# Performance work log

Hardware: AMD Instinct MI355X
Metric: run time of the kernel (lower is better)

Reference implementation:

```python
import jax, jax.numpy as jnp
import numpy as np

N = 50000   # nodes
E = 300000  # edges
D = 256     # emb_dim
L = 5       # num_layers
BN_EPS = 1e-5


def setup_inputs() -> dict:
    key = jax.random.key(0)
    ks = jax.random.split(key, 6)
    scale = 0.05
    return {
        "x": jax.random.normal(ks[0], (N, D), jnp.float32),
        "src": jax.random.randint(ks[1], (E,), 0, N, dtype=jnp.int32),
        "dst": jax.random.randint(ks[2], (E,), 0, N, dtype=jnp.int32),
        "W1": jax.random.normal(ks[3], (L, D, D), jnp.float32) * scale,
        "b1": jnp.zeros((L, D), jnp.float32),
        "g1": jnp.ones((L, D), jnp.float32),
        "bt1": jnp.zeros((L, D), jnp.float32),
        "W2": jax.random.normal(ks[4], (L, D, D), jnp.float32) * scale,
        "b2": jnp.zeros((L, D), jnp.float32),
        "eps": jnp.zeros((L,), jnp.float32),
        "bn_g": jnp.ones((L, D), jnp.float32),
        "bn_b": jnp.zeros((L, D), jnp.float32),
    }


def _bn(h, gamma, beta):
    # torch BatchNorm1d training-mode forward: biased batch stats over nodes
    mean = jnp.mean(h, axis=0)
    var = jnp.var(h, axis=0)
    return (h - mean) * jax.lax.rsqrt(var + BN_EPS) * gamma + beta


def reference(x, src, dst, W1, b1, g1, bt1, W2, b2, eps, bn_g, bn_b):
    h = x
    for l in range(L):
        # GINConv: gather relu(x[src]) -> scatter-sum to dst
        msg = jax.nn.relu(h[src])                          # [E, D]
        agg = jax.ops.segment_sum(msg, dst, num_segments=N)  # [N, D]
        z = (1.0 + eps[l]) * h + agg
        # mlp: Linear -> BN -> ReLU -> Linear
        z = z @ W1[l] + b1[l]
        z = jax.nn.relu(_bn(z, g1[l], bt1[l]))
        z = z @ W2[l] + b2[l]
        # per-layer BatchNorm; dropout is identity (eval / drop_ratio=0)
        z = _bn(z, bn_g[l], bn_b[l])
        if l < L - 1:
            z = jax.nn.relu(z)
        h = z
    return h  # JK='last'
```

## Files before the change

kernel.cpp:

```cpp
#include <hip/hip_runtime.h>
#include <hip/hip_bf16.h>

#define N_NODES 50000
#define N_EDGES 300000
#define DIM 256
#define MPAD 50048

typedef __attribute__((ext_vector_type(8))) _Float16 half8;
typedef __attribute__((ext_vector_type(4))) _Float16 half4;
typedef __attribute__((ext_vector_type(4))) float f32x4;

__device__ __forceinline__ void async16(const void* g, void* l) {
    __builtin_amdgcn_global_load_lds(
        (const __attribute__((address_space(1))) unsigned int*)g,
        (__attribute__((address_space(3))) unsigned int*)l, 16, 0, 0);
}

__device__ __forceinline__ void bn_finalize_thread(const float* __restrict__ st,
                                                   const float* __restrict__ g,
                                                   const float* __restrict__ beta,
                                                   float* scshL, int d, int n) {
    float s = 0.0f, sq = 0.0f;
#pragma unroll
    for (int r = 0; r < 8; r++) {
        s += st[r * 512 + d];
        sq += st[r * 512 + 256 + d];
    }
    float invn = 1.0f / (float)n;
    float mean = s * invn;
    float var = sq * invn - mean * mean;
    float inv = rsqrtf(var + 1e-5f);
    float scale = g[d] * inv;
    scshL[d] = scale;
    scshL[256 + d] = beta[d] - mean * scale;
}

__global__ __launch_bounds__(256) void hist_dst(const int* __restrict__ dst,
                                                int* __restrict__ deg, int E) {
    int e = blockIdx.x * blockDim.x + threadIdx.x;
    if (e < E) atomicAdd(&deg[dst[e]], 1);
}

__global__ __launch_bounds__(1024) void scan_blk(const int* __restrict__ deg,
                                                 int* __restrict__ ptr,
                                                 int* __restrict__ bsum, int n) {
    __shared__ int wsum[16];
    __shared__ int wpre[16];
    int tid = threadIdx.x;
    int i = blockIdx.x * 1024 + tid;
    int v = (i < n) ? deg[i] : 0;
    int lane = tid & 63, w = tid >> 6;
    int s = v;
#pragma unroll
    for (int off = 1; off < 64; off <<= 1) {
        int t = __shfl_up(s, off, 64);
        if (lane >= off) s += t;
    }
    if (lane == 63) wsum[w] = s;
    __syncthreads();
    if (tid < 16) {
        int acc = 0;
        for (int j = 0; j < tid; j++) acc += wsum[j];
        wpre[tid] = acc;
    }
    __syncthreads();
    int incl = s + wpre[w];
    if (i < n) ptr[i] = incl - v;
    if (tid == 1023) bsum[blockIdx.x] = incl;
}

__global__ __launch_bounds__(1024) void scan_add(int* __restrict__ ptr,
                                                 const int* __restrict__ bsum,
                                                 int* __restrict__ cursor,
                                                 int n, int E) {
    __shared__ int soff;
    int tid = threadIdx.x;
    if (tid < 64) {
        int v = (tid < (int)blockIdx.x) ? bsum[tid] : 0;
#pragma unroll
        for (int off = 32; off > 0; off >>= 1) v += __shfl_down(v, off, 64);
        if (tid == 0) soff = v;
    }
    __syncthreads();
    int i = blockIdx.x * 1024 + tid;
    if (i < n) {
        int val = ptr[i] + soff;
        ptr[i] = val;
        cursor[i] = val;
    }
    if (i == n) ptr[n] = E;
}

__global__ __launch_bounds__(256) void scatter_src(const int* __restrict__ src,
                                                   const int* __restrict__ dst,
                                                   int* __restrict__ cursor,
                                                   int* __restrict__ srcbuf, int E) {
    int e = blockIdx.x * blockDim.x + threadIdx.x;
    if (e < E) {
        int pos = atomicAdd(&cursor[dst[e]], 1);
        srcbuf[pos] = src[e];
    }
}

__global__ __launch_bounds__(256) void prep(const float* __restrict__ W1,
                                            const float* __restrict__ W2,
                                            _Float16* __restrict__ Wt,
                                            const float* __restrict__ x,
                                            _Float16* __restrict__ hb) {
    __shared__ float tile[64][65];
    int tid = threadIdx.x;
    if (blockIdx.x < 160) {
        int mat = blockIdx.x >> 4;
        int t = blockIdx.x & 15;
        int tr = t >> 2, tc = t & 3;
        const float* W = (mat < 5) ? (W1 + (size_t)mat * 65536)
                                   : (W2 + (size_t)(mat - 5) * 65536);
        int c = tid & 63, r0 = tid >> 6;
#pragma unroll 4
        for (int i = 0; i < 16; i++) {
            int r = r0 + i * 4;
            tile[r][c] = W[(size_t)(tr * 64 + r) * 256 + tc * 64 + c];
        }
        __syncthreads();
        _Float16* o = Wt + (size_t)mat * 65536;
#pragma unroll 4
        for (int i = 0; i < 16; i++) {
            int r = r0 + i * 4;
            o[(size_t)(tc * 64 + r) * 256 + tr * 64 + c] = (_Float16)tile[c][r];
        }
    } else {
        size_t i = (size_t)(blockIdx.x - 160) * 256 + tid;
        float4 v = ((const float4*)x)[i];
        half4 o;
        o.x = (_Float16)v.x; o.y = (_Float16)v.y;
        o.z = (_Float16)v.z; o.w = (_Float16)v.w;
        ((half4*)hb)[i] = o;
    }
}

__global__ __launch_bounds__(256) void gather_h(const _Float16* __restrict__ h,
                                                const int* __restrict__ ptr,
                                                const int* __restrict__ srcbuf,
                                                _Float16* __restrict__ z,
                                                const float* __restrict__ eps) {
    int node = blockIdx.x * 4 + (threadIdx.x >> 6);
    if (node >= N_NODES) return;
    int lane = threadIdx.x & 63;
    int beg = ptr[node], end = ptr[node + 1];
    float s = 1.0f + eps[0];
    half4 hv = ((const half4*)(h + (size_t)node * DIM))[lane];
    float a0 = (float)hv.x * s, a1 = (float)hv.y * s;
    float a2 = (float)hv.z * s, a3 = (float)hv.w * s;
    int e = beg;
    for (; e + 4 <= end; e += 4) {
        int s0 = srcbuf[e], s1 = srcbuf[e + 1], s2 = srcbuf[e + 2], s3 = srcbuf[e + 3];
        half4 v0 = ((const half4*)(h + (size_t)s0 * DIM))[lane];
        half4 v1 = ((const half4*)(h + (size_t)s1 * DIM))[lane];
        half4 v2 = ((const half4*)(h + (size_t)s2 * DIM))[lane];
        half4 v3 = ((const half4*)(h + (size_t)s3 * DIM))[lane];
        a0 += fmaxf((float)v0.x, 0.f) + fmaxf((float)v1.x, 0.f)
            + fmaxf((float)v2.x, 0.f) + fmaxf((float)v3.x, 0.f);
        a1 += fmaxf((float)v0.y, 0.f) + fmaxf((float)v1.y, 0.f)
            + fmaxf((float)v2.y, 0.f) + fmaxf((float)v3.y, 0.f);
        a2 += fmaxf((float)v0.z, 0.f) + fmaxf((float)v1.z, 0.f)
            + fmaxf((float)v2.z, 0.f) + fmaxf((float)v3.z, 0.f);
        a3 += fmaxf((float)v0.w, 0.f) + fmaxf((float)v1.w, 0.f)
            + fmaxf((float)v2.w, 0.f) + fmaxf((float)v3.w, 0.f);
    }
    for (; e < end; e++) {
        half4 v = ((const half4*)(h + (size_t)srcbuf[e] * DIM))[lane];
        a0 += fmaxf((float)v.x, 0.f); a1 += fmaxf((float)v.y, 0.f);
        a2 += fmaxf((float)v.z, 0.f); a3 += fmaxf((float)v.w, 0.f);
    }
    half4 o;
    o.x = (_Float16)a0; o.y = (_Float16)a1;
    o.z = (_Float16)a2; o.w = (_Float16)a3;
    ((half4*)(z + (size_t)node * DIM))[lane] = o;
}

__global__ __launch_bounds__(256) void gather_bn(const _Float16* __restrict__ C,
                                                 const int* __restrict__ ptr,
                                                 const int* __restrict__ srcbuf,
                                                 _Float16* __restrict__ z,
                                                 const float* __restrict__ scsh,
                                                 const float* __restrict__ eps,
                                                 int l) {
    int node = blockIdx.x * 4 + (threadIdx.x >> 6);
    if (node >= N_NODES) return;
    int lane = threadIdx.x & 63;
    float4 sc = ((const float4*)scsh)[lane];
    float4 sh = ((const float4*)(scsh + DIM))[lane];
    int beg = ptr[node], end = ptr[node + 1];
    float s = 1.0f + eps[l];
    half4 hv = ((const half4*)(C + (size_t)node * DIM))[lane];
    float a0 = s * fmaxf((float)hv.x * sc.x + sh.x, 0.f);
    float a1 = s * fmaxf((float)hv.y * sc.y + sh.y, 0.f);
    float a2 = s * fmaxf((float)hv.z * sc.z + sh.z, 0.f);
    float a3 = s * fmaxf((float)hv.w * sc.w + sh.w, 0.f);
    int e = beg;
    for (; e + 4 <= end; e += 4) {
        int s0 = srcbuf[e], s1 = srcbuf[e + 1], s2 = srcbuf[e + 2], s3 = srcbuf[e + 3];
        half4 v0 = ((const half4*)(C + (size_t)s0 * DIM))[lane];
        half4 v1 = ((const half4*)(C + (size_t)s1 * DIM))[lane];
        half4 v2 = ((const half4*)(C + (size_t)s2 * DIM))[lane];
        half4 v3 = ((const half4*)(C + (size_t)s3 * DIM))[lane];
        a0 += fmaxf((float)v0.x * sc.x + sh.x, 0.f) + fmaxf((float)v1.x * sc.x + sh.x, 0.f)
            + fmaxf((float)v2.x * sc.x + sh.x, 0.f) + fmaxf((float)v3.x * sc.x + sh.x, 0.f);
        a1 += fmaxf((float)v0.y * sc.y + sh.y, 0.f) + fmaxf((float)v1.y * sc.y + sh.y, 0.f)
            + fmaxf((float)v2.y * sc.y + sh.y, 0.f) + fmaxf((float)v3.y * sc.y + sh.y, 0.f);
        a2 += fmaxf((float)v0.z * sc.z + sh.z, 0.f) + fmaxf((float)v1.z * sc.z + sh.z, 0.f)
            + fmaxf((float)v2.z * sc.z + sh.z, 0.f) + fmaxf((float)v3.z * sc.z + sh.z, 0.f);
        a3 += fmaxf((float)v0.w * sc.w + sh.w, 0.f) + fmaxf((float)v1.w * sc.w + sh.w, 0.f)
            + fmaxf((float)v2.w * sc.w + sh.w, 0.f) + fmaxf((float)v3.w * sc.w + sh.w, 0.f);
    }
    for (; e < end; e++) {
        half4 v = ((const half4*)(C + (size_t)srcbuf[e] * DIM))[lane];
        a0 += fmaxf((float)v.x * sc.x + sh.x, 0.f);
        a1 += fmaxf((float)v.y * sc.y + sh.y, 0.f);
        a2 += fmaxf((float)v.z * sc.z + sh.z, 0.f);
        a3 += fmaxf((float)v.w * sc.w + sh.w, 0.f);
    }
    half4 o;
    o.x = (_Float16)a0; o.y = (_Float16)a1;
    o.z = (_Float16)a2; o.w = (_Float16)a3;
    ((half4*)(z + (size_t)node * DIM))[lane] = o;
}

#define GEMM_EPILOGUE                                                        \
    __syncthreads();                                                         \
    float* colsum = (float*)((char*)smem + 34816);                           \
    float* colsq = colsum + 128;                                             \
    if (tid < 128) { colsum[tid] = 0.0f; colsq[tid] = 0.0f; }                \
    _Float16* Cs = (_Float16*)smem;                                          \
    float bcol[4];                                                           \
    _Pragma("unroll")                                                        \
    for (int j = 0; j < 4; j++) bcol[j] = bias[col0 + wn + j * 16 + lrow];   \
    float csum[4] = {0.f, 0.f, 0.f, 0.f};                                    \
    float csq[4] = {0.f, 0.f, 0.f, 0.f};                                     \
    _Pragma("unroll")                                                        \
    for (int i = 0; i < 4; i++) {                                            \
        int rl = wm + i * 16 + quad * 4;                                     \
        _Pragma("unroll")                                                    \
        for (int j = 0; j < 4; j++) {                                        \
            int cl = wn + j * 16 + lrow;                                     \
            _Pragma("unroll")                                                \
            for (int r = 0; r < 4; r++) {                                    \
                float v = acc[i][j][r] + bcol[j];                            \
                Cs[(rl + r) * 136 + cl] = (_Float16)v;                       \
                if (row0 + rl + r < M) { csum[j] += v; csq[j] += v * v; }    \
            }                                                                \
        }                                                                    \
    }                                                                        \
    __syncthreads();                                                         \
    {                                                                        \
        int rgrp = lane >> 4, ch = lane & 15;                                \
        _Pragma("unroll")                                                    \
        for (int it = 0; it < 8; it++) {                                     \
            int row = wid * 32 + it * 4 + rgrp;                              \
            uint4 vv = *(const uint4*)(Cs + row * 136 + ch * 8);             \
            *(uint4*)(C + (size_t)(row0 + row) * DIM + col0 + ch * 8) = vv;  \
        }                                                                    \
    }                                                                        \
    _Pragma("unroll")                                                        \
    for (int j = 0; j < 4; j++) {                                            \
        atomicAdd(&colsum[wn + j * 16 + lrow], csum[j]);                     \
        atomicAdd(&colsq[wn + j * 16 + lrow], csq[j]);                       \
    }                                                                        \
    __syncthreads();                                                         \
    if (tid < 128) {                                                         \
        float* st = stats + (blockIdx.y & 7) * 512;                          \
        atomicAdd(&st[col0 + tid], colsum[tid]);                             \
        atomicAdd(&st[DIM + col0 + tid], colsq[tid]);                        \
    }

__global__ __launch_bounds__(256) void gemm_f16(const _Float16* __restrict__ A,
                                                const _Float16* __restrict__ Wt,
                                                const float* __restrict__ bias,
                                                _Float16* __restrict__ C,
                                                float* __restrict__ stats,
                                                int M) {
    __shared__ uint4 smem[2240];

    int tid = threadIdx.x;
    int wid = tid >> 6, lane = tid & 63;
    int quad = lane >> 4, lrow = lane & 15;
    int row0 = blockIdx.y * 128, col0 = blockIdx.x * 128;
    int wm = (wid & 1) * 64, wn = (wid >> 1) * 64;

    f32x4 acc[4][4] = {};
    const char* Ab = (const char*)A;
    const char* Bb = (const char*)Wt;

#pragma unroll
    for (int ko = 0; ko < 4; ko++) {
        int kb0 = ko * 128;
#pragma unroll
        for (int j = 0; j < 4; j++) {
            int sbase = wid * 256 + j * 64;
            int s = sbase + lane;
            int m = s >> 3;
            int c = (s & 7) ^ (m & 7);
            size_t go = (size_t)(row0 + m) * 512 + kb0 + c * 16;
            async16(Ab + go, (char*)smem + sbase * 16);
            size_t gob = (size_t)(col0 + m) * 512 + kb0 + c * 16;
            async16(Bb + gob, (char*)smem + 16384 + sbase * 16);
        }
        __syncthreads();
#pragma unroll
        for (int kc = 0; kc < 2; kc++) {
            half8 af[4], bf[4];
#pragma unroll
            for (int t = 0; t < 4; t++) {
                int ma = wm + t * 16 + lrow;
                int ca = kc * 4 + quad;
                af[t] = *(const half8*)((const char*)smem +
                                        (ma * 8 + (ca ^ (ma & 7))) * 16);
                int mb = wn + t * 16 + lrow;
                bf[t] = *(const half8*)((const char*)smem + 16384 +
                                        (mb * 8 + (ca ^ (mb & 7))) * 16);
            }
#pragma unroll
            for (int i = 0; i < 4; i++)
#pragma unroll
                for (int j2 = 0; j2 < 4; j2++)
                    acc[i][j2] = __builtin_amdgcn_mfma_f32_16x16x32_f16(
                        af[i], bf[j2], acc[i][j2], 0, 0, 0);
        }
        if (ko < 3) __syncthreads();
    }

    GEMM_EPILOGUE
}

__global__ __launch_bounds__(256) void gemm_bn(const _Float16* __restrict__ A,
                                               const _Float16* __restrict__ Wt,
                                               const float* __restrict__ bias,
                                               _Float16* __restrict__ C,
                                               float* __restrict__ stats,
                                               const float* __restrict__ statsIn,
                                               const float* __restrict__ gamma1,
                                               const float* __restrict__ beta1,
                                               int M) {
    __shared__ uint4 smem[2368];

    int tid = threadIdx.x;
    int wid = tid >> 6, lane = tid & 63;
    int quad = lane >> 4, lrow = lane & 15;
    int row0 = blockIdx.y * 128, col0 = blockIdx.x * 128;
    int wm = (wid & 1) * 64, wn = (wid >> 1) * 64;

    float* scshL = (float*)((char*)smem + 35840);
    bn_finalize_thread(statsIn, gamma1, beta1, scshL, tid, M);
    __syncthreads();

    half8 scv[8], shv[8];
#pragma unroll
    for (int cc = 0; cc < 8; cc++) {
        int kk = cc * 32 + quad * 8;
        float4 s0 = *(const float4*)(scshL + kk);
        float4 s1 = *(const float4*)(scshL + kk + 4);
        float4 h0 = *(const float4*)(scshL + DIM + kk);
        float4 h1 = *(const float4*)(scshL + DIM + kk + 4);
        half8 sv = {(_Float16)s0.x, (_Float16)s0.y, (_Float16)s0.z, (_Float16)s0.w,
                    (_Float16)s1.x, (_Float16)s1.y, (_Float16)s1.z, (_Float16)s1.w};
        half8 hv = {(_Float16)h0.x, (_Float16)h0.y, (_Float16)h0.z, (_Float16)h0.w,
                    (_Float16)h1.x, (_Float16)h1.y, (_Float16)h1.z, (_Float16)h1.w};
        scv[cc] = sv;
        shv[cc] = hv;
    }

    f32x4 acc[4][4] = {};
    const char* Ab = (const char*)A;
    const char* Bb = (const char*)Wt;
    const half8 zerov = {0, 0, 0, 0, 0, 0, 0, 0};

#pragma unroll
    for (int ko = 0; ko < 4; ko++) {
        int kb0 = ko * 128;
#pragma unroll
        for (int j = 0; j < 4; j++) {
            int sbase = wid * 256 + j * 64;
            int s = sbase + lane;
            int m = s >> 3;
            int c = (s & 7) ^ (m & 7);
            size_t go = (size_t)(row0 + m) * 512 + kb0 + c * 16;
            async16(Ab + go, (char*)smem + sbase * 16);
            size_t gob = (size_t)(col0 + m) * 512 + kb0 + c * 16;
            async16(Bb + gob, (char*)smem + 16384 + sbase * 16);
        }
        __syncthreads();
#pragma unroll
        for (int kc = 0; kc < 2; kc++) {
            half8 af[4], bf[4];
            half8 sv = scv[ko * 2 + kc];
            half8 hv = shv[ko * 2 + kc];
#pragma unroll
            for (int t = 0; t < 4; t++) {
                int ma = wm + t * 16 + lrow;
                int ca = kc * 4 + quad;
                half8 a = *(const half8*)((const char*)smem +
                                          (ma * 8 + (ca ^ (ma & 7))) * 16);
                af[t] = __builtin_elementwise_max(a * sv + hv, zerov);
                int mb = wn + t * 16 + lrow;
                bf[t] = *(const half8*)((const char*)smem + 16384 +
                                        (mb * 8 + (ca ^ (mb & 7))) * 16);
            }
#pragma unroll
            for (int i = 0; i < 4; i++)
#pragma unroll
                for (int j2 = 0; j2 < 4; j2++)
                    acc[i][j2] = __builtin_amdgcn_mfma_f32_16x16x32_f16(
                        af[i], bf[j2], acc[i][j2], 0, 0, 0);
        }
        if (ko < 3) __syncthreads();
    }

    GEMM_EPILOGUE
}

__global__ __launch_bounds__(256) void bn_finalize(const float* __restrict__ stats,
                                                   const float* __restrict__ g,
                                                   const float* __restrict__ beta,
                                                   float* __restrict__ scsh,
                                                   int n) {
    int d = threadIdx.x;
    float s = 0.0f, sq = 0.0f;
#pragma unroll
    for (int r = 0; r < 8; r++) {
        s += stats[r * 512 + d];
        sq += stats[r * 512 + 256 + d];
    }
    float invn = 1.0f / (float)n;
    float mean = s * invn;
    float var = sq * invn - mean * mean;
    float inv = rsqrtf(var + 1e-5f);
    float scale = g[d] * inv;
    scsh[d] = scale;
    scsh[DIM + d] = beta[d] - mean * scale;
}

__global__ __launch_bounds__(256) void bn_apply_f(const _Float16* __restrict__ in,
                                                  float* __restrict__ outf,
                                                  const float* __restrict__ scsh) {
    size_t i = (size_t)blockIdx.x * 256 + threadIdx.x;
    int c4 = (int)(i & 63);
    float4 sc = ((const float4*)scsh)[c4];
    float4 sh = ((const float4*)(scsh + DIM))[c4];
    half4 v = ((const half4*)in)[i];
    float4 o;
    o.x = (float)v.x * sc.x + sh.x;
    o.y = (float)v.y * sc.y + sh.y;
    o.z = (float)v.z * sc.z + sh.z;
    o.w = (float)v.w * sc.w + sh.w;
    ((float4*)outf)[i] = o;
}

extern "C" void kernel_launch(void* const* d_in, const int* in_sizes, int n_in,
                              void* d_out, int out_size, void* d_ws, size_t ws_size,
                              hipStream_t stream) {
    (void)in_sizes; (void)n_in; (void)out_size; (void)ws_size;
    const float* x   = (const float*)d_in[0];
    const int*   src = (const int*)d_in[1];
    const int*   dst = (const int*)d_in[2];
    const float* W1  = (const float*)d_in[3];
    const float* b1  = (const float*)d_in[4];
    const float* g1  = (const float*)d_in[5];
    const float* bt1 = (const float*)d_in[6];
    const float* W2  = (const float*)d_in[7];
    const float* b2  = (const float*)d_in[8];
    const float* eps = (const float*)d_in[9];
    const float* bng = (const float*)d_in[10];
    const float* bnb = (const float*)d_in[11];
    float* out = (float*)d_out;

    const int N = N_NODES, E = N_EDGES, D = DIM;
    size_t NDp = (size_t)MPAD * D;

    _Float16* gin  = (_Float16*)d_ws;
    _Float16* C1   = gin + NDp;
    _Float16* C2   = C1 + NDp;
    _Float16* Wt   = C2 + NDp;
    float* statsA  = (float*)(Wt + 10 * 65536);
    float* statsB  = statsA + 5 * 4096;
    int* deg       = (int*)(statsB + 5 * 4096);
    int* ptr       = deg + N;
    int* bsum      = ptr + N + 1;
    int* srcbuf    = bsum + 64;
    float* scshB   = (float*)(srcbuf + E);

    const int ELEM4_BLOCKS = N * D / 4 / 256;
    const int NODE_BLOCKS  = (N + 3) / 4;
    const int E_BLOCKS     = (E + 255) / 256;
    const int SCAN_BLOCKS  = (N + 1023) / 1024;
    const dim3 GEMM_GRID(2, MPAD / 128);

    hipMemsetAsync(statsA, 0, (size_t)(10 * 4096 + N) * sizeof(float), stream);
    hist_dst<<<E_BLOCKS, 256, 0, stream>>>(dst, deg, E);
    scan_blk<<<SCAN_BLOCKS, 1024, 0, stream>>>(deg, ptr, bsum, N);
    scan_add<<<SCAN_BLOCKS, 1024, 0, stream>>>(ptr, bsum, deg, N, E);
    scatter_src<<<E_BLOCKS, 256, 0, stream>>>(src, dst, deg, srcbuf, E);
    prep<<<160 + ELEM4_BLOCKS, 256, 0, stream>>>(W1, W2, Wt, x, C1);

    for (int l = 0; l < 5; l++) {
        float* stA = statsA + (size_t)l * 4096;
        float* stB = statsB + (size_t)l * 4096;

        if (l == 0)
            gather_h<<<NODE_BLOCKS, 256, 0, stream>>>(C1, ptr, srcbuf, gin, eps);
        else
            gather_bn<<<NODE_BLOCKS, 256, 0, stream>>>(C2, ptr, srcbuf, gin,
                                                       scshB, eps, l);

        gemm_f16<<<GEMM_GRID, 256, 0, stream>>>(
            gin, Wt + (size_t)l * 65536, b1 + (size_t)l * D, C1, stA, N);

        gemm_bn<<<GEMM_GRID, 256, 0, stream>>>(
            C1, Wt + (size_t)(5 + l) * 65536, b2 + (size_t)l * D, C2,
            stB, stA, g1 + (size_t)l * D, bt1 + (size_t)l * D, N);

        bn_finalize<<<1, 256, 0, stream>>>(stB, bng + (size_t)l * D,
                                           bnb + (size_t)l * D, scshB, N);

        if (l == 4)
            bn_apply_f<<<ELEM4_BLOCKS, 256, 0, stream>>>(C2, out, scshB);
    }
}
```

Before: 636.3 us.

## Double-buffer GEMM K-loop with 32-wide stages to overlap loads and MFMA

Both GEMM kernels now split K into eight 32-wide slices held in two LDS buffers. The async global-to-LDS load for the next slice is issued before the MFMAs on the current one, so the two can overlap. Before, each 128-wide chunk was loaded and then computed with no overlap. The cost is twice as many barriers, smaller stages, and a new 4-way XOR swizzle that may have more bank conflicts.

```diff
diff --git a/kernel.cpp b/kernel.cpp
--- a/kernel.cpp
+++ b/kernel.cpp
@@ -273,6 +273,19 @@
         atomicAdd(&st[DIM + col0 + tid], colsq[tid]);                        \
     }
 
+#define STAGE32(buf, k)                                                      \
+    _Pragma("unroll")                                                        \
+    for (int j = 0; j < 2; j++) {                                            \
+        int sbase = wid * 128 + j * 64;                                      \
+        int s = sbase + lane;                                                \
+        int m = s >> 2;                                                      \
+        int c = (s & 3) ^ (m & 3);                                           \
+        size_t go = (size_t)(row0 + m) * 512 + (k) * 64 + c * 16;            \
+        async16(Ab + go, (char*)smem + (buf) * 16384 + sbase * 16);          \
+        size_t gob = (size_t)(col0 + m) * 512 + (k) * 64 + c * 16;           \
+        async16(Bb + gob, (char*)smem + (buf) * 16384 + 8192 + sbase * 16);  \
+    }
+
 __global__ __launch_bounds__(256) void gemm_f16(const _Float16* __restrict__ A,
                                                 const _Float16* __restrict__ Wt,
                                                 const float* __restrict__ bias,
@@ -291,42 +304,29 @@
     const char* Ab = (const char*)A;
     const char* Bb = (const char*)Wt;
 
-#pragma unroll
-    for (int ko = 0; ko < 4; ko++) {
-        int kb0 = ko * 128;
-#pragma unroll
-        for (int j = 0; j < 4; j++) {
-            int sbase = wid * 256 + j * 64;
-            int s = sbase + lane;
-            int m = s >> 3;
-            int c = (s & 7) ^ (m & 7);
-            size_t go = (size_t)(row0 + m) * 512 + kb0 + c * 16;
-            async16(Ab + go, (char*)smem + sbase * 16);
-            size_t gob = (size_t)(col0 + m) * 512 + kb0 + c * 16;
-            async16(Bb + gob, (char*)smem + 16384 + sbase * 16);
+    STAGE32(0, 0);
+    __syncthreads();
+#pragma unroll
+    for (int k = 0; k < 8; k++) {
+        int buf = k & 1;
+        if (k < 7) STAGE32(buf ^ 1, k + 1);
+        half8 af[4], bf[4];
+#pragma unroll
+        for (int t = 0; t < 4; t++) {
+            int ma = wm + t * 16 + lrow;
+            af[t] = *(const half8*)((const char*)smem + buf * 16384 +
+                                    (ma * 4 + (quad ^ (ma & 3))) * 16);
+            int mb = wn + t * 16 + lrow;
+            bf[t] = *(const half8*)((const char*)smem + buf * 16384 + 8192 +
+                                    (mb * 4 + (quad ^ (mb & 3))) * 16);
         }
-        __syncthreads();
-#pragma unroll
-        for (int kc = 0; kc < 2; kc++) {
-            half8 af[4], bf[4];
-#pragma unroll
-            for (int t = 0; t < 4; t++) {
-                int ma = wm + t * 16 + lrow;
-                int ca = kc * 4 + quad;
-                af[t] = *(const half8*)((const char*)smem +
-                                        (ma * 8 + (ca ^ (ma & 7))) * 16);
-                int mb = wn + t * 16 + lrow;
-                bf[t] = *(const half8*)((const char*)smem + 16384 +
-                                        (mb * 8 + (ca ^ (mb & 7))) * 16);
-            }
-#pragma unroll
-            for (int i = 0; i < 4; i++)
-#pragma unroll
-                for (int j2 = 0; j2 < 4; j2++)
-                    acc[i][j2] = __builtin_amdgcn_mfma_f32_16x16x32_f16(
-                        af[i], bf[j2], acc[i][j2], 0, 0, 0);
-        }
-        if (ko < 3) __syncthreads();
+#pragma unroll
+        for (int i = 0; i < 4; i++)
+#pragma unroll
+            for (int j2 = 0; j2 < 4; j2++)
+                acc[i][j2] = __builtin_amdgcn_mfma_f32_16x16x32_f16(
+                    af[i], bf[j2], acc[i][j2], 0, 0, 0);
+        if (k < 7) __syncthreads();
     }
 
     GEMM_EPILOGUE
@@ -374,45 +374,32 @@
     const char* Bb = (const char*)Wt;
     const half8 zerov = {0, 0, 0, 0, 0, 0, 0, 0};
 
-#pragma unroll
-    for (int ko = 0; ko < 4; ko++) {
-        int kb0 = ko * 128;
-#pragma unroll
-        for (int j = 0; j < 4; j++) {
-            int sbase = wid * 256 + j * 64;
-            int s = sbase + lane;
-            int m = s >> 3;
-            int c = (s & 7) ^ (m & 7);
-            size_t go = (size_t)(row0 + m) * 512 + kb0 + c * 16;
-            async16(Ab + go, (char*)smem + sbase * 16);
-            size_t gob = (size_t)(col0 + m) * 512 + kb0 + c * 16;
-            async16(Bb + gob, (char*)smem + 16384 + sbase * 16);
+    STAGE32(0, 0);
+    __syncthreads();
+#pragma unroll
+    for (int k = 0; k < 8; k++) {
+        int buf = k & 1;
+        if (k < 7) STAGE32(buf ^ 1, k + 1);
+        half8 af[4], bf[4];
+        half8 sv = scv[k];
+        half8 hv = shv[k];
+#pragma unroll
+        for (int t = 0; t < 4; t++) {
+            int ma = wm + t * 16 + lrow;
+            half8 a = *(const half8*)((const char*)smem + buf * 16384 +
+                                      (ma * 4 + (quad ^ (ma & 3))) * 16);
+            af[t] = __builtin_elementwise_max(a * sv + hv, zerov);
+            int mb = wn + t * 16 + lrow;
+            bf[t] = *(const half8*)((const char*)smem + buf * 16384 + 8192 +
+                                    (mb * 4 + (quad ^ (mb & 3))) * 16);
         }
-        __syncthreads();
-#pragma unroll
-        for (int kc = 0; kc < 2; kc++) {
-            half8 af[4], bf[4];
-            half8 sv = scv[ko * 2 + kc];
-            half8 hv = shv[ko * 2 + kc];
-#pragma unroll
-            for (int t = 0; t < 4; t++) {
-                int ma = wm + t * 16 + lrow;
-                int ca = kc * 4 + quad;
-                half8 a = *(const half8*)((const char*)smem +
-                                          (ma * 8 + (ca ^ (ma & 7))) * 16);
-                af[t] = __builtin_elementwise_max(a * sv + hv, zerov);
-                int mb = wn + t * 16 + lrow;
-                bf[t] = *(const half8*)((const char*)smem + 16384 +
-                                        (mb * 8 + (ca ^ (mb & 7))) * 16);
-            }
-#pragma unroll
-            for (int i = 0; i < 4; i++)
-#pragma unroll
-                for (int j2 = 0; j2 < 4; j2++)
-                    acc[i][j2] = __builtin_amdgcn_mfma_f32_16x16x32_f16(
-                        af[i], bf[j2], acc[i][j2], 0, 0, 0);
-        }
-        if (ko < 3) __syncthreads();
+#pragma unroll
+        for (int i = 0; i < 4; i++)
+#pragma unroll
+            for (int j2 = 0; j2 < 4; j2++)
+                acc[i][j2] = __builtin_amdgcn_mfma_f32_16x16x32_f16(
+                    af[i], bf[j2], acc[i][j2], 0, 0, 0);
+        if (k < 7) __syncthreads();
     }
 
     GEMM_EPILOGUE
```

After: 627.0 us, median of 2. Within noise of the previous version (-1.5%).
